# Kernel tuning notes

Hardware: AMD Instinct MI355X
Metric: run time of the kernel (lower is better)

The kernel has to match this reference:

```python
import jax, jax.numpy as jnp
import numpy as np

B, D, T = 8, 256, 4096      # batch, latent dim, frames
NQ, K = 8, 1024             # num quantizers, codebook size


def setup_inputs() -> dict:
    key = jax.random.key(0)
    k1, k2 = jax.random.split(key)
    x = jax.random.normal(k1, (B, D, T), dtype=jnp.float32)
    codebooks = jax.random.normal(k2, (NQ, K, D), dtype=jnp.float32)
    return {"x": x, "codebooks": codebooks}


def _vq(residual, cb):
    """Single VQ stage: nearest-neighbor in cb, lookup, VQ loss.
    residual: [B, T, D], cb: [K, D]
    """
    sg = jax.lax.stop_gradient
    dots = jnp.einsum('btd,kd->btk', residual, cb)                 # [B,T,K]
    dist = (residual ** 2).sum(-1, keepdims=True) - 2.0 * dots + (cb ** 2).sum(-1)
    idx = jnp.argmin(dist, axis=-1)                                # [B,T]
    q = cb[idx]                                                    # gather [B,T,D]
    # commitment loss + codebook loss (standard VQ-VAE combination)
    loss = jnp.mean((sg(q) - residual) ** 2) + jnp.mean((q - sg(residual)) ** 2)
    return q, idx, loss


def reference(x, codebooks):
    """Residual VQ forward (eval mode, train=False).
    x: [B, D, T]; codebooks: [NQ, K, D]
    Returns (quantized_out [B,T,D], indices [NQ,B,T], losses [NQ]).
    """
    residual0 = jnp.transpose(x, (0, 2, 1))                        # [B,T,D]

    def step(carry, cb):
        res, qout = carry
        q, idx, loss = _vq(res, cb)
        q = jax.lax.stop_gradient(q)
        return (res - q, qout + q), (idx, loss)

    (_, quantized_out), (indices, losses) = jax.lax.scan(
        step, (residual0, jnp.zeros_like(residual0)), codebooks)
    return quantized_out, indices, losses
```

## Files before the change

### kernel.cpp

```cpp
#include <hip/hip_runtime.h>

#define B_   8
#define D_   256
#define T_   4096
#define NQ_  8
#define K_   1024

#define IDX_OFF  ((size_t)B_ * T_ * D_)
#define LOSS_OFF (IDX_OFF + (size_t)NQ_ * B_ * T_)

#define XT_OFF   0ull
#define CB16_OFF 33554432ull
#define CN_OFF   37748736ull
#define LB_OFF   37781504ull

typedef _Float16 half8 __attribute__((ext_vector_type(8)));
typedef float   f32x16 __attribute__((ext_vector_type(16)));

__device__ __forceinline__ ushort f2h(float f) {
  return __builtin_bit_cast(ushort, (_Float16)f);
}

__device__ __forceinline__ float packsc(float sc, uint code) {
  return __builtin_bit_cast(float, (__builtin_bit_cast(uint, sc) & ~1023u) | code);
}
__device__ __forceinline__ void ins3(float& v1, float& v2, float& v3, float f) {
  const float a1 = fminf(v1, f), b1 = fmaxf(v1, f);
  v1 = a1;
  const float a2 = fminf(v2, b1), b2 = fmaxf(v2, b1);
  v2 = a2;
  v3 = fminf(v3, b2);
}

__global__ void prep_xT(const float* __restrict__ x, float* __restrict__ xT) {
  __shared__ float tile[64][65];
  const int bidx = blockIdx.x;
  const int b = bidx >> 8, dc = (bidx >> 6) & 3, tc = bidx & 63;
  const int d0 = dc * 64, t0 = tc * 64;
  const int tid = threadIdx.x;
  {
    const int tt = tid & 63, dg = tid >> 6;
    for (int i = 0; i < 16; ++i) {
      const int d = dg * 16 + i;
      tile[d][tt] = x[((size_t)(b * D_ + d0 + d)) * T_ + t0 + tt];
    }
  }
  __syncthreads();
  {
    const int dw = tid & 63, tg = tid >> 6;
    for (int i = 0; i < 16; ++i) {
      const int t = tg * 16 + i;
      xT[((size_t)b * T_ + t0 + t) * D_ + d0 + dw] = tile[dw][t];
    }
  }
}

__global__ void prep_cb16(const float* __restrict__ cb, ushort* __restrict__ cb16,
                          float* __restrict__ cnorm) {
  const int tid = threadIdx.x, w = tid >> 6, l = tid & 63;
  const int code = blockIdx.x * 4 + w;
  const int s = code >> 10, ci = code & 1023, tile = ci >> 5, n = ci & 31;
  const float* row = cb + (size_t)code * D_;
  const float4 v = *(const float4*)(row + l * 4);
  double nrm = (double)v.x * v.x + (double)v.y * v.y + (double)v.z * v.z + (double)v.w * v.w;
  ushort4 p;
  p.x = f2h(v.x); p.y = f2h(v.y); p.z = f2h(v.z); p.w = f2h(v.w);
  const int ks = l >> 2, lf = ((l >> 1) & 1) * 32 + n, j0 = (l & 1) * 4;
  const size_t off = (((size_t)s * 32 + tile) * 16 + ks) * 512 + (size_t)lf * 8 + j0;
  *(ushort4*)(cb16 + off) = p;
#pragma unroll
  for (int m = 1; m <= 32; m <<= 1) nrm += __shfl_xor(nrm, m);
  if (l == 0) cnorm[code] = (float)nrm;
}

__global__ __launch_bounds__(256)
void rvq_main(const float* __restrict__ cb, const float* __restrict__ xT,
              const ushort* __restrict__ cb16, const float* __restrict__ cnorm,
              float* __restrict__ out, double* __restrict__ lossbuf) {
  __shared__ __align__(16) uint4  res16[1024];
  __shared__ float candm[32][12];

  const int tid = threadIdx.x;
  const int w = tid >> 6, l = tid & 63, n5 = l & 31, h = l >> 5;
  const size_t row0 = (size_t)blockIdx.x * 32;
  const int rowL = tid >> 3;
  const int dq = tid & 7;

  float res[4][8];

  {
#pragma unroll
    for (int cc = 0; cc < 4; ++cc) {
      const int kb = dq * 4 + cc;
      const float* xp = xT + (row0 + rowL) * D_ + kb * 8;
      const float4 x0 = *(const float4*)xp, x1 = *(const float4*)(xp + 4);
      res[cc][0] = x0.x; res[cc][1] = x0.y; res[cc][2] = x0.z; res[cc][3] = x0.w;
      res[cc][4] = x1.x; res[cc][5] = x1.y; res[cc][6] = x1.z; res[cc][7] = x1.w;
      uint4 pv;
      pv.x = __builtin_bit_cast(uint, __builtin_amdgcn_cvt_pkrtz(x0.x, x0.y));
      pv.y = __builtin_bit_cast(uint, __builtin_amdgcn_cvt_pkrtz(x0.z, x0.w));
      pv.z = __builtin_bit_cast(uint, __builtin_amdgcn_cvt_pkrtz(x1.x, x1.y));
      pv.w = __builtin_bit_cast(uint, __builtin_amdgcn_cvt_pkrtz(x1.z, x1.w));
      res16[kb * 32 + (rowL ^ dq)] = pv;
    }
  }
  __syncthreads();

  for (int s = 0; s < NQ_; ++s) {
    float v1 = 3e38f, v2 = 3e38f, v3 = 3e38f;
    float u1 = 3e38f, u2 = 3e38f, u3 = 3e38f;
    for (int tt = 0; tt < 8; ++tt) {
      const int t = w * 8 + tt;
      const uint4* ap = (const uint4*)(cb16 + ((size_t)(s * 32 + t) * 16) * 512) + l;
      int zr = 0;
      asm volatile("" : "+v"(zr));
      const uint4* bp = res16 + zr;
      f32x16 acc;
#pragma unroll
      for (int r = 0; r < 16; ++r) acc[r] = 0.0f;
#pragma unroll
      for (int q = 0; q < 4; ++q) {
        uint4 av[4], bv[4];
#pragma unroll
        for (int c = 0; c < 4; ++c) {
          const int ks = q * 4 + c;
          av[c] = ap[(size_t)ks * 64];
          bv[c] = bp[(ks * 2 + h) * 32 + (n5 ^ ((ks >> 1) & 7))];
        }
#pragma unroll
        for (int c = 0; c < 4; ++c) {
          acc = __builtin_amdgcn_mfma_f32_32x32x16_f16(
              __builtin_bit_cast(half8, av[c]), __builtin_bit_cast(half8, bv[c]), acc, 0, 0, 0);
        }
      }
      const float* cnb = cnorm + s * K_ + t * 32 + h * 4;
      const uint cbase = (uint)(t * 32 + 4 * h);
#pragma unroll
      for (int q = 0; q < 4; ++q) {
        const float4 cq = *(const float4*)(cnb + q * 8);
        const float cna[4] = {cq.x, cq.y, cq.z, cq.w};
#pragma unroll
        for (int rr = 0; rr < 4; ++rr) {
          const int r = q * 4 + rr;
          const float sc = cna[rr] - 2.0f * acc[r];
          const uint code = cbase + (uint)(8 * q + rr);
          const float f = packsc(sc, code);
          if (rr & 1) ins3(u1, u2, u3, f);
          else        ins3(v1, v2, v3, f);
        }
      }
    }
    ins3(v1, v2, v3, u1);
    ins3(v1, v2, v3, u2);
    ins3(v1, v2, v3, u3);
    {
      const float o1 = __shfl_xor(v1, 32), o2 = __shfl_xor(v2, 32), o3 = __shfl_xor(v3, 32);
      ins3(v1, v2, v3, o1);
      ins3(v1, v2, v3, o2);
      ins3(v1, v2, v3, o3);
    }
    if (h == 0) {
      candm[n5][w * 3 + 0] = v1;
      candm[n5][w * 3 + 1] = v2;
      candm[n5][w * 3 + 2] = v3;
    }
    __syncthreads();

    double lossW = 0.0;
    {
      float m1 = 3e38f, m2 = 3e38f, m3 = 3e38f;
#pragma unroll
      for (int cd = 0; cd < 12; ++cd) ins3(m1, m2, m3, candm[rowL][cd]);
      const int c1 = (int)(__builtin_bit_cast(uint, m1) & 1023u);
      const int c2 = (int)(__builtin_bit_cast(uint, m2) & 1023u);
      const int c3 = (int)(__builtin_bit_cast(uint, m3) & 1023u);

      const float* cbs = cb + (size_t)s * K_ * D_;
      const float* cr0 = cbs + (size_t)c1 * D_;
      const float* cr1 = cbs + (size_t)c2 * D_;
      const float* cr2 = cbs + (size_t)c3 * D_;
      double dd0 = 0.0, dd1 = 0.0, dd2 = 0.0;
#pragma unroll
      for (int cc = 0; cc < 4; ++cc) {
        const int kb = dq * 4 + cc;
        const int go = kb * 8;
        const float4 a0 = *(const float4*)(cr0 + go), a1 = *(const float4*)(cr0 + go + 4);
        const float4 b0 = *(const float4*)(cr1 + go), b1 = *(const float4*)(cr1 + go + 4);
        const float4 g0 = *(const float4*)(cr2 + go), g1 = *(const float4*)(cr2 + go + 4);
        const float af[8] = {a0.x, a0.y, a0.z, a0.w, a1.x, a1.y, a1.z, a1.w};
        const float bf[8] = {b0.x, b0.y, b0.z, b0.w, b1.x, b1.y, b1.z, b1.w};
        const float gf[8] = {g0.x, g0.y, g0.z, g0.w, g1.x, g1.y, g1.z, g1.w};
#pragma unroll
        for (int j = 0; j < 8; ++j) {
          const double r64 = (double)res[cc][j];
          const double u = r64 - (double)af[j]; dd0 += u * u;
          const double v = r64 - (double)bf[j]; dd1 += v * v;
          const double g = r64 - (double)gf[j]; dd2 += g * g;
        }
      }
#pragma unroll
      for (int m = 1; m <= 4; m <<= 1) {
        dd0 += __shfl_xor(dd0, m); dd1 += __shfl_xor(dd1, m); dd2 += __shfl_xor(dd2, m);
      }
      int win = c1; double dwn = dd0;
      if (dd1 < dwn || (dd1 == dwn && c2 < win)) { win = c2; dwn = dd1; }
      if (dd2 < dwn || (dd2 == dwn && c3 < win)) { win = c3; dwn = dd2; }
      const float* crw = cbs + (size_t)win * D_;
#pragma unroll
      for (int cc = 0; cc < 4; ++cc) {
        const int kb = dq * 4 + cc;
        const int go = kb * 8;
        const float4 w0 = *(const float4*)(crw + go), w1 = *(const float4*)(crw + go + 4);
        const float wf[8] = {w0.x, w0.y, w0.z, w0.w, w1.x, w1.y, w1.z, w1.w};
        if (s < NQ_ - 1) {
#pragma unroll
          for (int j = 0; j < 8; ++j) res[cc][j] = res[cc][j] - wf[j];
          uint4 pv;
          pv.x = __builtin_bit_cast(uint, __builtin_amdgcn_cvt_pkrtz(res[cc][0], res[cc][1]));
          pv.y = __builtin_bit_cast(uint, __builtin_amdgcn_cvt_pkrtz(res[cc][2], res[cc][3]));
          pv.z = __builtin_bit_cast(uint, __builtin_amdgcn_cvt_pkrtz(res[cc][4], res[cc][5]));
          pv.w = __builtin_bit_cast(uint, __builtin_amdgcn_cvt_pkrtz(res[cc][6], res[cc][7]));
          res16[kb * 32 + (rowL ^ dq)] = pv;
        } else {
          const float* xp = xT + (row0 + rowL) * D_ + go;
          const float4 x0 = *(const float4*)xp, x1 = *(const float4*)(xp + 4);
          const float xf[8] = {x0.x, x0.y, x0.z, x0.w, x1.x, x1.y, x1.z, x1.w};
          float o[8];
#pragma unroll
          for (int j = 0; j < 8; ++j) o[j] = xf[j] - (res[cc][j] - wf[j]);
          float* od = out + (row0 + rowL) * D_ + go;
          *(float4*)od       = make_float4(o[0], o[1], o[2], o[3]);
          *(float4*)(od + 4) = make_float4(o[4], o[5], o[6], o[7]);
        }
      }
      if (dq == 0) {
        out[IDX_OFF + (size_t)s * (B_ * T_) + row0 + rowL] = (float)win;
        lossW = dwn;
      }
    }
#pragma unroll
    for (int m = 8; m <= 32; m <<= 1) lossW += __shfl_xor(lossW, m);
    if (l == 0) atomicAdd(&lossbuf[s], lossW);
    __syncthreads();
  }
}

__global__ void rvq_loss(const double* __restrict__ lossbuf, float* __restrict__ out) {
  const int s = threadIdx.x;
  if (s < NQ_) out[LOSS_OFF + s] = (float)(2.0 * lossbuf[s] / (double)((size_t)B_ * T_ * D_));
}

extern "C" void kernel_launch(void* const* d_in, const int* in_sizes, int n_in,
                              void* d_out, int out_size, void* d_ws, size_t ws_size,
                              hipStream_t stream) {
  const float* x  = (const float*)d_in[0];
  const float* cb = (const float*)d_in[1];
  float* out = (float*)d_out;
  char* ws = (char*)d_ws;
  float*  xTp   = (float*)(ws + XT_OFF);
  ushort* cb16p = (ushort*)(ws + CB16_OFF);
  float*  cnp   = (float*)(ws + CN_OFF);
  double* lbp   = (double*)(ws + LB_OFF);

  hipMemsetAsync(ws + LB_OFF, 0, NQ_ * sizeof(double), stream);
  prep_xT<<<2048, 256, 0, stream>>>(x, xTp);
  prep_cb16<<<2048, 256, 0, stream>>>(cb, cb16p, cnp);
  rvq_main<<<1024, 256, 0, stream>>>(cb, xTp, cb16p, cnp, out, lbp);
  rvq_loss<<<1, 64, 0, stream>>>(lbp, out);
}
```

Baseline: 590.5 us.

## Software-pipeline codebook loads and hoist residual fragments into registers for MFMA loop

Restructures the per-stage distance loop into a fully unrolled 32-step sequence. Codebook fragments are prefetched two steps ahead through a three-slot register ring, and the residual B-operand fragments are loaded from LDS once per stage instead of once per tile. The top-3 insertion now uses fmed3 instead of a min/max chain, and the score uses an fma. The goal is to hide global load latency behind MFMA work and cut redundant LDS reads, at the cost of many more live registers (64 VGPRs for the B fragments plus the prefetch buffers) and a possible drop in occupancy.

Measured after the change: 590.3 us. Within noise of the previous version (-0.0%).

```diff
diff --git a/kernel.cpp b/kernel.cpp
--- a/kernel.cpp
+++ b/kernel.cpp
@@ -25,11 +25,12 @@
   return __builtin_bit_cast(float, (__builtin_bit_cast(uint, sc) & ~1023u) | code);
 }
 __device__ __forceinline__ void ins3(float& v1, float& v2, float& v3, float f) {
-  const float a1 = fminf(v1, f), b1 = fmaxf(v1, f);
-  v1 = a1;
-  const float a2 = fminf(v2, b1), b2 = fmaxf(v2, b1);
-  v2 = a2;
-  v3 = fminf(v3, b2);
+  const float a = v1;
+  const float m = fmaxf(v1, f);
+  v1 = fminf(v1, f);
+  const float v2n = __builtin_amdgcn_fmed3f(a, v2, f);
+  v3 = __builtin_amdgcn_fmed3f(v2, v3, m);
+  v2 = v2n;
 }
 
 __global__ void prep_xT(const float* __restrict__ x, float* __restrict__ xT) {
@@ -107,46 +108,59 @@
   __syncthreads();
 
   for (int s = 0; s < NQ_; ++s) {
+    const uint4* ap0 = (const uint4*)(cb16 + ((size_t)(s * 32 + w * 8) * 16) * 512) + l;
+    uint4 pa[3][4];
+#pragma unroll
+    for (int c = 0; c < 4; ++c) pa[0][c] = ap0[c * 64];
+#pragma unroll
+    for (int c = 0; c < 4; ++c) pa[1][c] = ap0[(4 + c) * 64];
+    half8 b[16];
+#pragma unroll
+    for (int ks = 0; ks < 16; ++ks) {
+      const uint4 bv = res16[(ks * 2 + h) * 32 + (n5 ^ ((ks >> 1) & 7))];
+      b[ks] = __builtin_bit_cast(half8, bv);
+    }
+
     float v1 = 3e38f, v2 = 3e38f, v3 = 3e38f;
     float u1 = 3e38f, u2 = 3e38f, u3 = 3e38f;
-    for (int tt = 0; tt < 8; ++tt) {
-      const int t = w * 8 + tt;
-      const uint4* ap = (const uint4*)(cb16 + ((size_t)(s * 32 + t) * 16) * 512) + l;
-      int zr = 0;
-      asm volatile("" : "+v"(zr));
-      const uint4* bp = res16 + zr;
-      f32x16 acc;
-#pragma unroll
-      for (int r = 0; r < 16; ++r) acc[r] = 0.0f;
-#pragma unroll
-      for (int q = 0; q < 4; ++q) {
-        uint4 av[4], bv[4];
-#pragma unroll
-        for (int c = 0; c < 4; ++c) {
-          const int ks = q * 4 + c;
-          av[c] = ap[(size_t)ks * 64];
-          bv[c] = bp[(ks * 2 + h) * 32 + (n5 ^ ((ks >> 1) & 7))];
-        }
-#pragma unroll
-        for (int c = 0; c < 4; ++c) {
-          acc = __builtin_amdgcn_mfma_f32_32x32x16_f16(
-              __builtin_bit_cast(half8, av[c]), __builtin_bit_cast(half8, bv[c]), acc, 0, 0, 0);
-        }
-      }
-      const float* cnb = cnorm + s * K_ + t * 32 + h * 4;
-      const uint cbase = (uint)(t * 32 + 4 * h);
-#pragma unroll
-      for (int q = 0; q < 4; ++q) {
-        const float4 cq = *(const float4*)(cnb + q * 8);
-        const float cna[4] = {cq.x, cq.y, cq.z, cq.w};
-#pragma unroll
-        for (int rr = 0; rr < 4; ++rr) {
-          const int r = q * 4 + rr;
-          const float sc = cna[rr] - 2.0f * acc[r];
-          const uint code = cbase + (uint)(8 * q + rr);
-          const float f = packsc(sc, code);
-          if (rr & 1) ins3(u1, u2, u3, f);
-          else        ins3(v1, v2, v3, f);
+    f32x16 acc;
+    float4 cq[4];
+#pragma unroll
+    for (int i = 0; i < 32; ++i) {
+      const int tt = i >> 2, q = i & 3;
+      if (q == 0) {
+        const float* cnb = cnorm + s * K_ + (w * 8 + tt) * 32 + h * 4;
+        cq[0] = *(const float4*)(cnb);
+        cq[1] = *(const float4*)(cnb + 8);
+        cq[2] = *(const float4*)(cnb + 16);
+        cq[3] = *(const float4*)(cnb + 24);
+#pragma unroll
+        for (int r = 0; r < 16; ++r) acc[r] = 0.0f;
+      }
+      if (i + 2 < 32) {
+        const int i2 = i + 2, t2 = i2 >> 2, q2 = i2 & 3, s2 = i2 % 3;
+#pragma unroll
+        for (int c = 0; c < 4; ++c) pa[s2][c] = ap0[t2 * 1024 + (q2 * 4 + c) * 64];
+      }
+      const int sl = i % 3;
+#pragma unroll
+      for (int c = 0; c < 4; ++c) {
+        acc = __builtin_amdgcn_mfma_f32_32x32x16_f16(
+            __builtin_bit_cast(half8, pa[sl][c]), b[q * 4 + c], acc, 0, 0, 0);
+      }
+      if (q == 3) {
+        const uint cbase = (uint)((w * 8 + tt) * 32 + 4 * h);
+#pragma unroll
+        for (int qq = 0; qq < 4; ++qq) {
+          const float cna[4] = {cq[qq].x, cq[qq].y, cq[qq].z, cq[qq].w};
+#pragma unroll
+          for (int rr = 0; rr < 4; ++rr) {
+            const float sc = fmaf(-2.0f, acc[qq * 4 + rr], cna[rr]);
+            const uint code = cbase + (uint)(8 * qq + rr);
+            const float f = packsc(sc, code);
+            if (rr & 1) ins3(u1, u2, u3, f);
+            else        ins3(v1, v2, v3, f);
+          }
         }
       }
     }
@@ -195,7 +209,7 @@
           const double r64 = (double)res[cc][j];
           const double u = r64 - (double)af[j]; dd0 += u * u;
           const double v = r64 - (double)bf[j]; dd1 += v * v;
-          const double g = r64 - (double)gf[j]; dd2 += g * g;
+          const double gg = r64 - (double)gf[j]; dd2 += gg * gg;
         }
       }
 #pragma unroll
```
